# Performance work log

Hardware: AMD Instinct MI355X
Metric: run time of the kernel (lower is better)

Reference implementation:

```python
import jax, jax.numpy as jnp
import numpy as np

EPS = 1e-10


def setup_inputs() -> dict:
    key = jax.random.key(0)
    k1, k2, k3, k4, k5, k6 = jax.random.split(key, 6)
    B, C, F = 128, 20000, 64
    return {
        "query": jax.random.normal(k1, (B, F), dtype=jnp.float32),
        "cases": jax.random.normal(k2, (C, F), dtype=jnp.float32),
        "case_labels": jax.random.normal(k3, (C,), dtype=jnp.float32),
        "w_fa": jax.random.uniform(k4, (F,), dtype=jnp.float32),
        "b_fa": jax.random.normal(k5, (F,), dtype=jnp.float32),
        "w_ca": jax.random.uniform(k6, (F,), dtype=jnp.float32),
        "b_ca": jnp.zeros((1,), dtype=jnp.float32),
        "top_k": 32,
    }


def reference(query, cases, case_labels, w_fa, b_fa, w_ca, b_ca, top_k):
    # Feature activations: per-feature similarity between each query and each case.
    # diff2: [B, C, F]
    diff2 = (query[:, None, :] - cases[None, :, :]) ** 2
    feature_activations = jax.nn.sigmoid(-diff2 * w_fa + b_fa)  # [B, C, F]

    # Case activations: shared linear reduction over features + sigmoid. [B, C]
    ca = jax.nn.sigmoid(jnp.einsum("bcf,f->bc", feature_activations, w_ca) + b_ca)

    # TopCaseLayer: keep only the top_k case activations per query, zero the rest.
    B = ca.shape[0]
    vals, idx = jax.lax.top_k(ca, top_k)  # [B, k]
    rows = jnp.arange(B)[:, None]
    ca_sel = jnp.zeros_like(ca).at[rows, idx].set(vals)

    # CustomSoftmaxLayer: divide by row sum (no exp).
    case_activations = ca_sel / (jnp.sum(ca_sel, axis=1, keepdims=True) + EPS)

    # Top-k gather on labels + mean (kNN-style output).
    _, idx2 = jax.lax.top_k(case_activations, top_k)
    output = jnp.mean(case_labels[idx2], axis=1)  # [B]

    predicted_number = case_activations @ case_labels  # [B]

    return (feature_activations, case_activations, output, predicted_number)
```

## Files before the change

kernel.cpp:

```cpp
#include <hip/hip_runtime.h>
#include <hip/hip_bf16.h>


#define EPS_DENOM 1e-10f

typedef float floatx4 __attribute__((ext_vector_type(4)));

#define NQ 8

__global__ __launch_bounds__(256) void fa_ca_kernel(
    const float* __restrict__ q,
    const float* __restrict__ cases,
    const float* __restrict__ w_fa,
    const float* __restrict__ b_fa,
    const float* __restrict__ w_ca,
    const float* __restrict__ b_ca,
    float* __restrict__ fa_out,
    float* __restrict__ ca_out,
    int B, int C)
{
    const int g  = threadIdx.x & 15;
    const int p  = threadIdx.x >> 4;
    const int b0 = blockIdx.y * NQ;
    const int c0 = blockIdx.x * 64 + p;
    const int f4 = g * 4;

    const float4 wf = *reinterpret_cast<const float4*>(w_fa + f4);
    const float4 bf = *reinterpret_cast<const float4*>(b_fa + f4);
    const float4 wc = *reinterpret_cast<const float4*>(w_ca + f4);
    const float  bca = b_ca[0];

    float4 qv[NQ];
    #pragma unroll
    for (int i = 0; i < NQ; ++i) {
        int bq = b0 + i;
        if (bq > B - 1) bq = B - 1;
        qv[i] = *reinterpret_cast<const float4*>(q + (size_t)bq * 64 + f4);
    }

    #pragma unroll
    for (int j = 0; j < 4; ++j) {
        const int c = c0 + j * 16;
        if (c >= C) break;

        const float4 cv = *reinterpret_cast<const float4*>(cases + (size_t)c * 64 + f4);

        #pragma unroll
        for (int i = 0; i < NQ; ++i) {
            const int b = b0 + i;
            if (b >= B) break;

            float d0 = qv[i].x - cv.x, d1 = qv[i].y - cv.y;
            float d2 = qv[i].z - cv.z, d3 = qv[i].w - cv.w;
            float s0 = 1.0f / (1.0f + __expf(fmaf(d0 * d0, wf.x, -bf.x)));
            float s1 = 1.0f / (1.0f + __expf(fmaf(d1 * d1, wf.y, -bf.y)));
            float s2 = 1.0f / (1.0f + __expf(fmaf(d2 * d2, wf.z, -bf.z)));
            float s3 = 1.0f / (1.0f + __expf(fmaf(d3 * d3, wf.w, -bf.w)));

            floatx4 sv = { s0, s1, s2, s3 };
            __builtin_nontemporal_store(
                sv, reinterpret_cast<floatx4*>(fa_out + ((size_t)b * C + c) * 64 + f4));

            float dot = s0 * wc.x + s1 * wc.y + s2 * wc.z + s3 * wc.w;
            dot += __shfl_xor(dot, 1, 64);
            dot += __shfl_xor(dot, 2, 64);
            dot += __shfl_xor(dot, 4, 64);
            dot += __shfl_xor(dot, 8, 64);

            if (g == 0) {
                float cav = 1.0f / (1.0f + __expf(-(dot + bca)));
                ca_out[(size_t)b * C + c] = cav;
            }
        }
    }
}

#define TPB3     1024
#define NWAVE    (TPB3 / 64)
#define NBINS    1024
#define NPRIV    8
#define CAND_CAP 2048
#define ROWCAP   20000

__global__ __launch_bounds__(TPB3) void topk_kernel4(
    float* __restrict__ ca,
    const float* __restrict__ labels,
    float* __restrict__ out_mean,
    float* __restrict__ out_pred,
    int C, const int* __restrict__ kp)
{
    __shared__ float    row_lds[ROWCAP];
    __shared__ unsigned histf[NBINS * NPRIV];
    __shared__ unsigned hist2[NBINS];
    __shared__ unsigned sc[NBINS];
    __shared__ unsigned cand_key[CAND_CAP];
    __shared__ int      cand_idx[CAND_CAP];
    __shared__ float    s_wa[NWAVE], s_wb[NWAVE];
    __shared__ float    s_resA;
    __shared__ int      s_cand_cnt;
    __shared__ unsigned s_bsel;
    __shared__ int      s_thr_hi, s_thr_lo;

    const int b    = blockIdx.x;
    const int t    = threadIdx.x;
    const int w    = t >> 6;
    const int lane = t & 63;
    float* rowg = ca + (size_t)b * C;

    int K = *kp;
    if (K < 1) K = 1;
    if (K > 256) K = 256;

    #pragma unroll
    for (int r = 0; r < NPRIV; ++r) histf[r * NBINS + t] = 0;
    __syncthreads();

    const int priv = w & (NPRIV - 1);
    for (int i = t; i < C; i += TPB3) {
        float v = rowg[i];
        row_lds[i] = v;
        atomicAdd(&histf[(__float_as_uint(v) >> 21) * NPRIV + priv], 1u);
    }
    __syncthreads();

    {
        unsigned hm = 0;
        #pragma unroll
        for (int r = 0; r < NPRIV; ++r) hm += histf[t * NPRIV + r];
        hist2[t] = hm;
    }
    __syncthreads();

    unsigned prefix = 0, pmask = 0;
    int R = K;
    int cnt_bin = 0;
    const int shifts[3] = {21, 11, 1};

    for (int lvl = 0; lvl < 3; ++lvl) {
        const int shift = shifts[lvl];
        if (lvl > 0) {
            hist2[t] = 0;
            __syncthreads();
            for (int i = t; i < C; i += TPB3) {
                unsigned key = __float_as_uint(row_lds[i]);
                if ((key & pmask) == prefix)
                    atomicAdd(&hist2[(key >> shift) & (NBINS - 1u)], 1u);
            }
            __syncthreads();
        }
        if (w == 0) {
            unsigned v16[16], locsuf[16];
            #pragma unroll
            for (int m = 0; m < 16; ++m) v16[m] = hist2[lane * 16 + m];
            unsigned acc = 0;
            #pragma unroll
            for (int m = 15; m >= 0; --m) { acc += v16[m]; locsuf[m] = acc; }
            const unsigned lanetot = acc;
            unsigned suf = lanetot;
            #pragma unroll
            for (int off = 1; off < 64; off <<= 1) {
                unsigned o = __shfl_down(suf, (unsigned)off, 64);
                if (lane + off < 64) suf += o;
            }
            const unsigned baseh = suf - lanetot;
            #pragma unroll
            for (int m = 0; m < 16; ++m) sc[lane * 16 + m] = baseh + locsuf[m];
        }
        __syncthreads();
        {
            unsigned inc    = sc[t];
            unsigned strict = (t < NBINS - 1) ? sc[t + 1] : 0u;
            if ((int)strict < R && R <= (int)inc) s_bsel = (unsigned)t;
        }
        __syncthreads();
        const unsigned bsel       = s_bsel;
        const unsigned strict_sel = (bsel < NBINS - 1) ? sc[bsel + 1] : 0u;
        cnt_bin = (int)(sc[bsel] - strict_sel);
        R      -= (int)strict_sel;
        prefix |= bsel << shift;
        pmask  |= (NBINS - 1u) << shift;
        __syncthreads();
        if (cnt_bin <= CAND_CAP) break;
    }

    const bool tieflood = (cnt_bin > CAND_CAP);
    float my_selsum = 0.0f;
    bool sel0 = false, sel1 = false;
    unsigned k0 = 0, k1 = 0;
    int i0 = 0x7FFFFFFF, i1 = 0x7FFFFFFF;

    if (!tieflood) {
        if (t == 0) s_cand_cnt = 0;
        __syncthreads();
        for (int ib = 0; ib < C; ib += TPB3) {
            const int i = ib + t;
            bool is_cand = false;
            unsigned key = 0;
            if (i < C) {
                float v = row_lds[i];
                key = __float_as_uint(v);
                unsigned mk = key & pmask;
                if (mk > prefix)        my_selsum += v;
                else if (mk == prefix)  is_cand = true;
            }
            unsigned long long m = __ballot(is_cand);
            if (m) {
                const int ldr = (int)(__ffsll((unsigned long long)m) - 1);
                int base = 0;
                if (lane == ldr) base = atomicAdd(&s_cand_cnt, __popcll(m));
                base = __shfl(base, ldr, 64);
                if (is_cand) {
                    int pos = base + (int)__popcll(m & ((1ull << lane) - 1ull));
                    if (pos < CAND_CAP) { cand_key[pos] = key; cand_idx[pos] = i; }
                }
            }
        }
        __syncthreads();
        const int n_c = (s_cand_cnt < CAND_CAP) ? s_cand_cnt : CAND_CAP;
        if (t < n_c)        { k0 = cand_key[t];        i0 = cand_idx[t]; }
        if (t + TPB3 < n_c) { k1 = cand_key[t + TPB3]; i1 = cand_idx[t + TPB3]; }
        int r0 = 0, r1 = 0;
        for (int j = 0; j < n_c; ++j) {
            unsigned kj = cand_key[j];
            int      ij = cand_idx[j];
            r0 += (kj > k0 || (kj == k0 && ij < i0)) ? 1 : 0;
            r1 += (kj > k1 || (kj == k1 && ij < i1)) ? 1 : 0;
        }
        sel0 = (t < n_c) && (r0 < R);
        sel1 = (t + TPB3 < n_c) && (r1 < R);
        if (sel0) my_selsum += __uint_as_float(k0);
        if (sel1) my_selsum += __uint_as_float(k1);
    } else {
        if (t == 0) {
            int n1 = 0;
            for (int i = 0; i < C; ++i) {
                unsigned key = __float_as_uint(row_lds[i]);
                if ((key & pmask) == prefix && (key & 1u)) n1++;
            }
            int thr_hi = -1, thr_lo = -1;
            if (R <= n1) {
                int cnt = 0;
                for (int i = 0; i < C; ++i) {
                    unsigned key = __float_as_uint(row_lds[i]);
                    if ((key & pmask) == prefix && (key & 1u))
                        if (++cnt == R) { thr_hi = i; break; }
                }
            } else {
                thr_hi = C;
                int need = R - n1, cnt = 0;
                for (int i = 0; i < C; ++i) {
                    unsigned key = __float_as_uint(row_lds[i]);
                    if ((key & pmask) == prefix && !(key & 1u))
                        if (++cnt == need) { thr_lo = i; break; }
                }
            }
            s_thr_hi = thr_hi; s_thr_lo = thr_lo;
        }
        __syncthreads();
        const int thr_hi = s_thr_hi, thr_lo = s_thr_lo;
        for (int i = t; i < C; i += TPB3) {
            float v = row_lds[i];
            unsigned key = __float_as_uint(v);
            unsigned mk  = key & pmask;
            bool sel = (mk > prefix) ||
                       (mk == prefix && ((key & 1u) ? (i <= thr_hi) : (i <= thr_lo)));
            if (sel) my_selsum += v;
        }
    }

    {
        float a = my_selsum;
        #pragma unroll
        for (int off = 1; off < 64; off <<= 1) a += __shfl_xor(a, off, 64);
        if (lane == 0) s_wa[w] = a;
        __syncthreads();
        if (w == 0) {
            float x = (lane < NWAVE) ? s_wa[lane] : 0.0f;
            #pragma unroll
            for (int off = 1; off < NWAVE; off <<= 1) x += __shfl_xor(x, off, 64);
            if (lane == 0) s_resA = x;
        }
        __syncthreads();
    }
    const float denom = s_resA + EPS_DENOM;
    __syncthreads();

    float lsum = 0.0f, psum = 0.0f;
    const int thr_hi2 = tieflood ? s_thr_hi : 0;
    const int thr_lo2 = tieflood ? s_thr_lo : 0;
    for (int i = t; i < C; i += TPB3) {
        float v = row_lds[i];
        unsigned key = __float_as_uint(v);
        unsigned mk  = key & pmask;
        bool sel = (mk > prefix);
        if (tieflood && !sel && mk == prefix)
            sel = (key & 1u) ? (i <= thr_hi2) : (i <= thr_lo2);
        float outv = 0.0f;
        if (sel) {
            outv = v / denom;
            float lab = labels[i];
            lsum += lab;
            psum += outv * lab;
        }
        rowg[i] = outv;
    }
    __syncthreads();
    if (!tieflood) {
        if (sel0) {
            float ov = __uint_as_float(k0) / denom;
            rowg[i0] = ov;
            float lab = labels[i0];
            lsum += lab; psum += ov * lab;
        }
        if (sel1) {
            float ov = __uint_as_float(k1) / denom;
            rowg[i1] = ov;
            float lab = labels[i1];
            lsum += lab; psum += ov * lab;
        }
    }
    {
        float a = lsum, bb = psum;
        #pragma unroll
        for (int off = 1; off < 64; off <<= 1) {
            a  += __shfl_xor(a,  off, 64);
            bb += __shfl_xor(bb, off, 64);
        }
        if (lane == 0) { s_wa[w] = a; s_wb[w] = bb; }
        __syncthreads();
        if (w == 0) {
            float x = (lane < NWAVE) ? s_wa[lane] : 0.0f;
            float y = (lane < NWAVE) ? s_wb[lane] : 0.0f;
            #pragma unroll
            for (int off = 1; off < NWAVE; off <<= 1) {
                x += __shfl_xor(x, off, 64);
                y += __shfl_xor(y, off, 64);
            }
            if (lane == 0) {
                out_mean[b] = x / (float)K;
                out_pred[b] = y;
            }
        }
    }
}

extern "C" void kernel_launch(void* const* d_in, const int* in_sizes, int n_in,
                              void* d_out, int out_size, void* d_ws, size_t ws_size,
                              hipStream_t stream) {
    const float* q      = (const float*)d_in[0];
    const float* cases  = (const float*)d_in[1];
    const float* labels = (const float*)d_in[2];
    const float* w_fa   = (const float*)d_in[3];
    const float* b_fa   = (const float*)d_in[4];
    const float* w_ca   = (const float*)d_in[5];
    const float* b_ca   = (const float*)d_in[6];
    const int*   kp     = (const int*)d_in[7];

    const int F = in_sizes[3];
    const int B = in_sizes[0] / F;
    const int C = in_sizes[1] / F;

    float* out      = (float*)d_out;
    const size_t FA = (size_t)B * C * F;
    float* fa_out   = out;
    float* ca_out   = out + FA;
    float* out_mean = ca_out + (size_t)B * C;
    float* out_pred = out_mean + B;

    dim3 g1((C + 63) / 64, (B + NQ - 1) / NQ);
    fa_ca_kernel<<<g1, 256, 0, stream>>>(q, cases, w_fa, b_fa, w_ca, b_ca,
                                         fa_out, ca_out, B, C);
    topk_kernel4<<<B, TPB3, 0, stream>>>(ca_out, labels, out_mean, out_pred,
                                         C, kp);
}
```

Measured before the change: 187.9 us.

## Switch feature-activation kernel to grid-stride persistent blocks over single-query chunks

Replaces the 2D grid in which each block handled 8 queries by 64 cases with a fixed grid of 2048 blocks that loop over (query, 64-case) chunks. Each chunk now covers one query, so a block writes one contiguous 16KB span of the feature-activation output instead of 8 spans strided by C. The aim is better write streaming and fewer block launches. The cost is that each case vector is now reloaded once per query rather than shared across 8 queries, which raises L2 read traffic.

```diff
diff --git a/kernel.cpp b/kernel.cpp
--- a/kernel.cpp
+++ b/kernel.cpp
@@ -6,9 +6,7 @@
 
 typedef float floatx4 __attribute__((ext_vector_type(4)));
 
-#define NQ 8
-
-__global__ __launch_bounds__(256) void fa_ca_kernel(
+__global__ __launch_bounds__(256) void fa_ca_stream_kernel(
     const float* __restrict__ q,
     const float* __restrict__ cases,
     const float* __restrict__ w_fa,
@@ -17,12 +15,10 @@
     const float* __restrict__ b_ca,
     float* __restrict__ fa_out,
     float* __restrict__ ca_out,
-    int B, int C)
+    int B, int C, int CB )
 {
     const int g  = threadIdx.x & 15;
     const int p  = threadIdx.x >> 4;
-    const int b0 = blockIdx.y * NQ;
-    const int c0 = blockIdx.x * 64 + p;
     const int f4 = g * 4;
 
     const float4 wf = *reinterpret_cast<const float4*>(w_fa + f4);
@@ -30,28 +26,22 @@
     const float4 wc = *reinterpret_cast<const float4*>(w_ca + f4);
     const float  bca = b_ca[0];
 
-    float4 qv[NQ];
-    #pragma unroll
-    for (int i = 0; i < NQ; ++i) {
-        int bq = b0 + i;
-        if (bq > B - 1) bq = B - 1;
-        qv[i] = *reinterpret_cast<const float4*>(q + (size_t)bq * 64 + f4);
-    }
-
-    #pragma unroll
-    for (int j = 0; j < 4; ++j) {
-        const int c = c0 + j * 16;
-        if (c >= C) break;
-
-        const float4 cv = *reinterpret_cast<const float4*>(cases + (size_t)c * 64 + f4);
+    const int nchunks = B * CB;
+
+    for (int chunk = blockIdx.x; chunk < nchunks; chunk += gridDim.x) {
+        const int b  = chunk / CB;
+        const int c0 = (chunk - b * CB) * 64 + p;
+
+        const float4 qv = *reinterpret_cast<const float4*>(q + (size_t)b * 64 + f4);
 
         #pragma unroll
-        for (int i = 0; i < NQ; ++i) {
-            const int b = b0 + i;
-            if (b >= B) break;
-
-            float d0 = qv[i].x - cv.x, d1 = qv[i].y - cv.y;
-            float d2 = qv[i].z - cv.z, d3 = qv[i].w - cv.w;
+        for (int j = 0; j < 4; ++j) {
+            const int c = c0 + j * 16;
+            if (c >= C) break;
+
+            const float4 cv = *reinterpret_cast<const float4*>(cases + (size_t)c * 64 + f4);
+            float d0 = qv.x - cv.x, d1 = qv.y - cv.y;
+            float d2 = qv.z - cv.z, d3 = qv.w - cv.w;
             float s0 = 1.0f / (1.0f + __expf(fmaf(d0 * d0, wf.x, -bf.x)));
             float s1 = 1.0f / (1.0f + __expf(fmaf(d1 * d1, wf.y, -bf.y)));
             float s2 = 1.0f / (1.0f + __expf(fmaf(d2 * d2, wf.z, -bf.z)));
@@ -367,9 +357,10 @@
     float* out_mean = ca_out + (size_t)B * C;
     float* out_pred = out_mean + B;
 
-    dim3 g1((C + 63) / 64, (B + NQ - 1) / NQ);
-    fa_ca_kernel<<<g1, 256, 0, stream>>>(q, cases, w_fa, b_fa, w_ca, b_ca,
-                                         fa_out, ca_out, B, C);
+    const int CB = (C + 63) / 64;
+    const int grid1 = 2048;
+    fa_ca_stream_kernel<<<grid1, 256, 0, stream>>>(
+        q, cases, w_fa, b_fa, w_ca, b_ca, fa_out, ca_out, B, C, CB);
     topk_kernel4<<<B, TPB3, 0, stream>>>(ca_out, labels, out_mean, out_pred,
                                          C, kp);
 }
```

After: 231.2 us. 23.1% more time.
